# Optimization experiments

Hardware: AMD Instinct MI355X
Metric: run time of the kernel (lower is better)

The kernel has to match this reference:

```python
import jax, jax.numpy as jnp
import numpy as np

D = 1024          # feature_dim
ROT = D // 2      # rotary applied to first feature_dim//2 channels (RotaryEmbedding(dim//2))
B, S = 4, 8192


def _l2norm(x, eps=1e-6):
    # cos_sim feature map: x / ||x||_2 along feature dim
    return x * jax.lax.rsqrt(jnp.sum(x * x, axis=-1, keepdims=True) + eps)


def _rotary(x, rot_dim):
    # lucidrains rotary-embedding-torch: interleaved pairs, partial rotary on first rot_dim dims
    seq = x.shape[-2]
    half = rot_dim // 2
    inv_freq = 1.0 / (10000.0 ** (jnp.arange(0, rot_dim, 2, dtype=jnp.float32) / rot_dim))  # [rot/2]
    freqs = jnp.arange(seq, dtype=jnp.float32)[:, None] * inv_freq[None, :]                  # [s, rot/2]
    freqs = jnp.repeat(freqs, 2, axis=-1)                                                     # [s, rot]
    cos, sin = jnp.cos(freqs), jnp.sin(freqs)
    xr, xp = x[..., :rot_dim], x[..., rot_dim:]
    x2 = xr.reshape(*xr.shape[:-1], half, 2)
    rh = jnp.stack([-x2[..., 1], x2[..., 0]], axis=-1).reshape(xr.shape)  # rotate_half, interleaved
    return jnp.concatenate([xr * cos + rh * sin, xp], axis=-1)


def _layernorm(x, g, b, eps=1e-5):
    mu = jnp.mean(x, axis=-1, keepdims=True)
    var = jnp.mean(jnp.square(x - mu), axis=-1, keepdims=True)
    return (x - mu) * jax.lax.rsqrt(var + eps) * g + b


def setup_inputs() -> dict:
    key = jax.random.key(0)
    k1, k2, k3 = jax.random.split(key, 3)
    X = jax.random.normal(k1, (B, S, D), jnp.float32)
    W_in = jax.random.normal(k2, (3 * D, D), jnp.float32) / np.float32(np.sqrt(D))
    W_out = jax.random.normal(k3, (D, D), jnp.float32) / np.float32(np.sqrt(D))
    ln_g = jnp.ones((D,), jnp.float32)
    ln_b = jnp.zeros((D,), jnp.float32)
    return {"X": X, "W_in": W_in, "W_out": W_out, "ln_g": ln_g, "ln_b": ln_b}


def reference(X, W_in, W_out, ln_g, ln_b):
    Xn = _layernorm(X, ln_g, ln_b)
    QKV = jnp.einsum('bsd,ed->bse', Xn, W_in)        # in_proj, no bias
    Q, K, V = jnp.split(QKV, 3, axis=-1)
    Q = _rotary(Q, ROT)
    K = _rotary(K, ROT)
    A = jnp.sum(_l2norm(K) * V, axis=-2)             # [b, d] global feature-map reduction
    Y = A[:, None, :] * _l2norm(Q)                   # feature_map_attn = identity
    Y = jnp.einsum('bsd,ed->bse', Y, W_out)          # out_proj, no bias
    return Y + X                                     # residual
```

## Files before the change

kernel.cpp:

```cpp
#include <hip/hip_runtime.h>

#define D 1024
#define S_LEN 8192
#define BATCH 4
#define NROWS (BATCH * S_LEN)

typedef unsigned short u16;
typedef __attribute__((ext_vector_type(8))) short short8;
typedef __attribute__((ext_vector_type(8))) unsigned short u16x8;
typedef __attribute__((ext_vector_type(4))) unsigned short u16x4;
typedef __attribute__((ext_vector_type(4))) float f32x4;

__device__ __forceinline__ float bf2f(u16 u) {
  return __builtin_bit_cast(float, ((unsigned)u) << 16);
}
__device__ __forceinline__ u16 f2bf(float f) {
  unsigned u = __builtin_bit_cast(unsigned, f);
  u += 0x7FFFu + ((u >> 16) & 1u);
  return (u16)(u >> 16);
}

#define GLD16(gp, lp)                                                    \
  __builtin_amdgcn_global_load_lds(                                      \
      (__attribute__((address_space(1))) void*)(void*)(gp),              \
      (__attribute__((address_space(3))) void*)(void*)(lp), 16, 0, 0)

__global__ __launch_bounds__(256) void tobf16_kernel(
    const float* __restrict__ src, u16* __restrict__ dst, int n4) {
  int t = blockIdx.x * 256 + threadIdx.x;
  if (t < n4) {
    float4 v = *(const float4*)&src[(size_t)t * 4];
    u16x4 o;
    o[0] = f2bf(v.x); o[1] = f2bf(v.y); o[2] = f2bf(v.z); o[3] = f2bf(v.w);
    *(u16x4*)&dst[(size_t)t * 4] = o;
  }
}

__global__ __launch_bounds__(256) void rope_table_kernel(
    float* __restrict__ ct, float* __restrict__ st) {
  int t = blockIdx.x * 256 + threadIdx.x;
  int s = t >> 8, j = t & 255;
  float invf = exp2f((float)j * -0.0519051265f);
  float f = (float)s * invf;
  float sv, cv;
  sincosf(f, &sv, &cv);
  ct[t] = cv;
  st[t] = sv;
}

__global__ __launch_bounds__(256) void ln_kernel(
    const float* __restrict__ X, const float* __restrict__ g,
    const float* __restrict__ bb, u16* __restrict__ Xn) {
  const int wave = threadIdx.x >> 6, lane = threadIdx.x & 63;
  const int row = blockIdx.x * 4 + wave;
  const float* xr = X + (size_t)row * D;
  float4 v[4];
  float s = 0.f, sq = 0.f;
#pragma unroll
  for (int i = 0; i < 4; i++) {
    v[i] = *(const float4*)&xr[lane * 4 + i * 256];
    s += v[i].x + v[i].y + v[i].z + v[i].w;
    sq += v[i].x * v[i].x + v[i].y * v[i].y + v[i].z * v[i].z + v[i].w * v[i].w;
  }
#pragma unroll
  for (int off = 32; off > 0; off >>= 1) {
    s += __shfl_xor(s, off);
    sq += __shfl_xor(sq, off);
  }
  const float mu = s * (1.f / D);
  const float var = sq * (1.f / D) - mu * mu;
  const float rstd = rsqrtf(var + 1e-5f);
#pragma unroll
  for (int i = 0; i < 4; i++) {
    const int c = lane * 4 + i * 256;
    float4 gg = *(const float4*)&g[c];
    float4 bv = *(const float4*)&bb[c];
    u16x4 o;
    o[0] = f2bf((v[i].x - mu) * rstd * gg.x + bv.x);
    o[1] = f2bf((v[i].y - mu) * rstd * gg.y + bv.y);
    o[2] = f2bf((v[i].z - mu) * rstd * gg.z + bv.z);
    o[3] = f2bf((v[i].w - mu) * rstd * gg.w + bv.w);
    *(u16x4*)&Xn[(size_t)row * D + c] = o;
  }
}

template <int EPI>
__global__ __launch_bounds__(256) void gemm_bt(
    const u16* __restrict__ A, const u16* __restrict__ Bm,
    u16* __restrict__ Cbf, const float* __restrict__ Xres,
    float* __restrict__ Cf, int K, int ldc) {
  __shared__ u16 smem[2 * 128 * 64];
  u16* As = smem;
  u16* Bs = smem + 128 * 64;
  const int tid = threadIdx.x;
  const int wave = tid >> 6, lane = tid & 63;
  const int wm = wave >> 1, wn = wave & 1;
  const int l15 = lane & 15, quad = lane >> 4;
  const int m0 = blockIdx.y * 128;
  const int n0 = blockIdx.x * 128;
  const int sw = l15 & 7;

  f32x4 acc[4][4] = {};

  for (int k0 = 0; k0 < K; k0 += 64) {
    __syncthreads();
#pragma unroll
    for (int i = 0; i < 4; i++) {
      const int c = i * 256 + tid;
      const int row = c >> 3;
      const int g = (c & 7) ^ (row & 7);
      GLD16(&A[(size_t)(m0 + row) * K + k0 + g * 8], &As[c * 8]);
      GLD16(&Bm[(size_t)(n0 + row) * K + k0 + g * 8], &Bs[c * 8]);
    }
    __syncthreads();
#pragma unroll
    for (int ks = 0; ks < 2; ks++) {
      short8 af[4], bfr[4];
#pragma unroll
      for (int i = 0; i < 4; i++)
        af[i] = *(const short8*)
            &As[(wm * 64 + i * 16 + l15) * 64 + (((ks * 4 + quad) ^ sw) << 3)];
#pragma unroll
      for (int j = 0; j < 4; j++)
        bfr[j] = *(const short8*)
            &Bs[(wn * 64 + j * 16 + l15) * 64 + (((ks * 4 + quad) ^ sw) << 3)];
#pragma unroll
      for (int i = 0; i < 4; i++)
#pragma unroll
        for (int j = 0; j < 4; j++)
          acc[i][j] = __builtin_amdgcn_mfma_f32_16x16x32_bf16(
              af[i], bfr[j], acc[i][j], 0, 0, 0);
    }
  }

  if constexpr (EPI == 0) {
    __syncthreads();
    u16* my = smem + wave * 4096;
#pragma unroll
    for (int i = 0; i < 4; i++)
#pragma unroll
      for (int j = 0; j < 4; j++)
#pragma unroll
        for (int r = 0; r < 4; r++)
          my[(i * 16 + quad * 4 + r) * 64 + j * 16 + l15] = f2bf(acc[i][j][r]);
    __syncthreads();
#pragma unroll
    for (int t = 0; t < 8; t++) {
      const int flat = t * 512 + lane * 8;
      const int r64 = flat >> 6, c64 = flat & 63;
      *(u16x8*)&Cbf[(size_t)(m0 + wm * 64 + r64) * ldc + n0 + wn * 64 + c64] =
          *(const u16x8*)&my[flat];
    }
  } else {
#pragma unroll
    for (int i = 0; i < 4; i++) {
#pragma unroll
      for (int r = 0; r < 4; r++) {
        const int row = m0 + wm * 64 + i * 16 + quad * 4 + r;
#pragma unroll
        for (int j = 0; j < 4; j++) {
          const int col = n0 + wn * 64 + j * 16 + l15;
          Cf[(size_t)row * ldc + col] =
              acc[i][j][r] + Xres[(size_t)row * ldc + col];
        }
      }
    }
  }
}

__global__ __launch_bounds__(256) void areduce_kernel(
    const u16* __restrict__ QKV, const float* __restrict__ ct,
    const float* __restrict__ st, float* __restrict__ Aout) {
  const int wave = threadIdx.x >> 6, lane = threadIdx.x & 63;
  const int b = blockIdx.x >> 8;
  const int chunk = blockIdx.x & 255;
  const int c0 = lane << 4;
  float acc[16];
#pragma unroll
  for (int i = 0; i < 16; i++) acc[i] = 0.f;

  for (int t = 0; t < 8; t++) {
    const int s = chunk * 32 + wave * 8 + t;
    const size_t base = ((size_t)b * S_LEN + s) * (3 * D);
    u16x8 ka = *(const u16x8*)&QKV[base + D + c0];
    u16x8 kb = *(const u16x8*)&QKV[base + D + c0 + 8];
    float kx[16];
#pragma unroll
    for (int i = 0; i < 8; i++) { kx[i] = bf2f(ka[i]); kx[8 + i] = bf2f(kb[i]); }
    if (lane < 32) {
      const int jb = c0 >> 1;
      const float* cp = &ct[(size_t)s * 256 + jb];
      const float* sp = &st[(size_t)s * 256 + jb];
#pragma unroll
      for (int p = 0; p < 8; p++) {
        float cv = cp[p], sv = sp[p];
        float e = kx[2 * p], o = kx[2 * p + 1];
        kx[2 * p] = e * cv - o * sv;
        kx[2 * p + 1] = o * cv + e * sv;
      }
    }
    float sq = 0.f;
#pragma unroll
    for (int i = 0; i < 16; i++) sq += kx[i] * kx[i];
#pragma unroll
    for (int off = 32; off > 0; off >>= 1) sq += __shfl_xor(sq, off);
    const float rn = rsqrtf(sq + 1e-6f);
    u16x8 va = *(const u16x8*)&QKV[base + 2 * D + c0];
    u16x8 vb = *(const u16x8*)&QKV[base + 2 * D + c0 + 8];
#pragma unroll
    for (int i = 0; i < 8; i++) {
      acc[i] += kx[i] * rn * bf2f(va[i]);
      acc[8 + i] += kx[8 + i] * rn * bf2f(vb[i]);
    }
  }

  __shared__ float red[D];
  if (wave == 0) {
#pragma unroll
    for (int i = 0; i < 16; i++) red[c0 + i] = acc[i];
  }
  __syncthreads();
  for (int w = 1; w < 4; w++) {
    if (wave == w) {
#pragma unroll
      for (int i = 0; i < 16; i++) red[c0 + i] += acc[i];
    }
    __syncthreads();
  }
  const int tid = threadIdx.x;
#pragma unroll
  for (int i = 0; i < 4; i++)
    atomicAdd(&Aout[(b << 10) + tid * 4 + i], red[tid * 4 + i]);
}

__global__ __launch_bounds__(256) void y_kernel(
    const u16* __restrict__ QKV, const float* __restrict__ ct,
    const float* __restrict__ st, const float* __restrict__ Ain,
    u16* __restrict__ Y) {
  const int wave = threadIdx.x >> 6, lane = threadIdx.x & 63;
  const int row = blockIdx.x * 4 + wave;
  const int b = row >> 13, s = row & (S_LEN - 1);
  const int c0 = lane << 4;
  const size_t base = (size_t)row * (3 * D);
  u16x8 qa = *(const u16x8*)&QKV[base + c0];
  u16x8 qb = *(const u16x8*)&QKV[base + c0 + 8];
  float qx[16];
#pragma unroll
  for (int i = 0; i < 8; i++) { qx[i] = bf2f(qa[i]); qx[8 + i] = bf2f(qb[i]); }
  if (lane < 32) {
    const int jb = c0 >> 1;
    const float* cp = &ct[(size_t)s * 256 + jb];
    const float* sp = &st[(size_t)s * 256 + jb];
#pragma unroll
    for (int p = 0; p < 8; p++) {
      float cv = cp[p], sv = sp[p];
      float e = qx[2 * p], o = qx[2 * p + 1];
      qx[2 * p] = e * cv - o * sv;
      qx[2 * p + 1] = o * cv + e * sv;
    }
  }
  float sq = 0.f;
#pragma unroll
  for (int i = 0; i < 16; i++) sq += qx[i] * qx[i];
#pragma unroll
  for (int off = 32; off > 0; off >>= 1) sq += __shfl_xor(sq, off);
  const float rn = rsqrtf(sq + 1e-6f);
  u16x8 oa, ob;
#pragma unroll
  for (int i = 0; i < 8; i++) {
    oa[i] = f2bf(Ain[(b << 10) + c0 + i] * qx[i] * rn);
    ob[i] = f2bf(Ain[(b << 10) + c0 + 8 + i] * qx[8 + i] * rn);
  }
  *(u16x8*)&Y[(size_t)row * D + c0] = oa;
  *(u16x8*)&Y[(size_t)row * D + c0 + 8] = ob;
}

extern "C" void kernel_launch(void* const* d_in, const int* in_sizes, int n_in,
                              void* d_out, int out_size, void* d_ws, size_t ws_size,
                              hipStream_t stream) {
  const float* X = (const float*)d_in[0];
  const float* W_in = (const float*)d_in[1];
  const float* W_out = (const float*)d_in[2];
  const float* ln_g = (const float*)d_in[3];
  const float* ln_b = (const float*)d_in[4];
  float* out = (float*)d_out;

  char* ws = (char*)d_ws;
  size_t off = 0;
  auto alloc = [&](size_t bytes) -> void* {
    void* p = ws + off;
    off += (bytes + 255) & ~(size_t)255;
    return p;
  };
  u16* QKV = (u16*)alloc((size_t)NROWS * 3 * D * 2);
  u16* Xn = (u16*)alloc((size_t)NROWS * D * 2);
  u16* Yb = (u16*)alloc((size_t)NROWS * D * 2);
  u16* Winb = (u16*)alloc((size_t)3 * D * D * 2);
  u16* Woutb = (u16*)alloc((size_t)D * D * 2);
  float* ct = (float*)alloc((size_t)S_LEN * 256 * 4);
  float* st = (float*)alloc((size_t)S_LEN * 256 * 4);
  float* Aacc = (float*)alloc((size_t)BATCH * D * 4);

  hipMemsetAsync(Aacc, 0, (size_t)BATCH * D * 4, stream);
  tobf16_kernel<<<3 * D * D / 1024, 256, 0, stream>>>(W_in, Winb, 3 * D * D / 4);
  tobf16_kernel<<<D * D / 1024, 256, 0, stream>>>(W_out, Woutb, D * D / 4);
  rope_table_kernel<<<S_LEN, 256, 0, stream>>>(ct, st);
  ln_kernel<<<NROWS / 4, 256, 0, stream>>>(X, ln_g, ln_b, Xn);

  dim3 g1(3 * D / 128, NROWS / 128);
  gemm_bt<0><<<g1, 256, 0, stream>>>(Xn, Winb, QKV, nullptr, nullptr, D, 3 * D);

  areduce_kernel<<<BATCH * 256, 256, 0, stream>>>(QKV, ct, st, Aacc);
  y_kernel<<<NROWS / 4, 256, 0, stream>>>(QKV, ct, st, Aacc, Yb);

  dim3 g2(D / 128, NROWS / 128);
  gemm_bt<1><<<g2, 256, 0, stream>>>(Yb, Woutb, nullptr, X, out, D, D);
}
```

Measured before the change: 670.5 us.

## Coalesce GEMM residual epilogue via LDS, merge weight casts, stagger atomics

The out-projection epilogue now stages fp32 accumulators through shared memory in two halves, so the residual read and output write use contiguous float4 accesses instead of scattered scalar ones. The two weight bf16 conversion launches are merged into one, GEMM load addresses are precomputed and advanced by pointer increments, and the A-reduction atomics start at a per-block offset to spread contention. The costs are extra LDS traffic and an added barrier before the epilogue.

```diff
diff --git a/kernel.cpp b/kernel.cpp
--- a/kernel.cpp
+++ b/kernel.cpp
@@ -26,14 +26,24 @@
       (__attribute__((address_space(3))) void*)(void*)(lp), 16, 0, 0)
 
 __global__ __launch_bounds__(256) void tobf16_kernel(
-    const float* __restrict__ src, u16* __restrict__ dst, int n4) {
+    const float* __restrict__ a, u16* __restrict__ da, int n4a,
+    const float* __restrict__ b, u16* __restrict__ db, int n4b) {
   int t = blockIdx.x * 256 + threadIdx.x;
-  if (t < n4) {
-    float4 v = *(const float4*)&src[(size_t)t * 4];
-    u16x4 o;
-    o[0] = f2bf(v.x); o[1] = f2bf(v.y); o[2] = f2bf(v.z); o[3] = f2bf(v.w);
-    *(u16x4*)&dst[(size_t)t * 4] = o;
-  }
+  const float* s;
+  u16* d;
+  if (t < n4a) {
+    s = a + (size_t)t * 4;
+    d = da + (size_t)t * 4;
+  } else {
+    t -= n4a;
+    if (t >= n4b) return;
+    s = b + (size_t)t * 4;
+    d = db + (size_t)t * 4;
+  }
+  float4 v = *(const float4*)s;
+  u16x4 o;
+  o[0] = f2bf(v.x); o[1] = f2bf(v.y); o[2] = f2bf(v.z); o[3] = f2bf(v.w);
+  *(u16x4*)d = o;
 }
 
 __global__ __launch_bounds__(256) void rope_table_kernel(
@@ -100,17 +110,27 @@
   const int n0 = blockIdx.x * 128;
   const int sw = l15 & 7;
 
+  const u16* pa[4];
+  const u16* pb[4];
+#pragma unroll
+  for (int i = 0; i < 4; i++) {
+    const int c = i * 256 + tid;
+    const int row = c >> 3;
+    const int g = (c & 7) ^ (row & 7);
+    pa[i] = &A[(size_t)(m0 + row) * K + g * 8];
+    pb[i] = &Bm[(size_t)(n0 + row) * K + g * 8];
+  }
+
   f32x4 acc[4][4] = {};
 
   for (int k0 = 0; k0 < K; k0 += 64) {
     __syncthreads();
 #pragma unroll
     for (int i = 0; i < 4; i++) {
-      const int c = i * 256 + tid;
-      const int row = c >> 3;
-      const int g = (c & 7) ^ (row & 7);
-      GLD16(&A[(size_t)(m0 + row) * K + k0 + g * 8], &As[c * 8]);
-      GLD16(&Bm[(size_t)(n0 + row) * K + k0 + g * 8], &Bs[c * 8]);
+      GLD16(pa[i], &As[(i * 256 + tid) * 8]);
+      GLD16(pb[i], &Bs[(i * 256 + tid) * 8]);
+      pa[i] += 64;
+      pb[i] += 64;
     }
     __syncthreads();
 #pragma unroll
@@ -133,8 +153,8 @@
     }
   }
 
+  __syncthreads();
   if constexpr (EPI == 0) {
-    __syncthreads();
     u16* my = smem + wave * 4096;
 #pragma unroll
     for (int i = 0; i < 4; i++)
@@ -152,17 +172,29 @@
           *(const u16x8*)&my[flat];
     }
   } else {
-#pragma unroll
-    for (int i = 0; i < 4; i++) {
-#pragma unroll
-      for (int r = 0; r < 4; r++) {
-        const int row = m0 + wm * 64 + i * 16 + quad * 4 + r;
-#pragma unroll
-        for (int j = 0; j < 4; j++) {
-          const int col = n0 + wn * 64 + j * 16 + l15;
-          Cf[(size_t)row * ldc + col] =
-              acc[i][j][r] + Xres[(size_t)row * ldc + col];
-        }
+    float* fs = (float*)smem + wave * 2048;
+#pragma unroll
+    for (int h = 0; h < 2; h++) {
+#pragma unroll
+      for (int i = 0; i < 4; i++)
+#pragma unroll
+        for (int jj = 0; jj < 2; jj++)
+#pragma unroll
+          for (int r = 0; r < 4; r++)
+            fs[(i * 16 + quad * 4 + r) * 32 + jj * 16 + l15] =
+                acc[i][h * 2 + jj][r];
+#pragma unroll
+      for (int t = 0; t < 8; t++) {
+        const int f = t * 256 + lane * 4;
+        const int r64 = f >> 5, c32 = f & 31;
+        float4 v = *(const float4*)&fs[f];
+        const size_t row = m0 + wm * 64 + r64;
+        const size_t col = n0 + wn * 64 + h * 32 + c32;
+        float4 xr = *(const float4*)&Xres[row * ldc + col];
+        float4 o;
+        o.x = v.x + xr.x; o.y = v.y + xr.y;
+        o.z = v.z + xr.z; o.w = v.w + xr.w;
+        *(float4*)&Cf[row * ldc + col] = o;
       }
     }
   }
@@ -228,9 +260,10 @@
     __syncthreads();
   }
   const int tid = threadIdx.x;
+  const int start = (tid + blockIdx.x * 4) & 255;
 #pragma unroll
   for (int i = 0; i < 4; i++)
-    atomicAdd(&Aout[(b << 10) + tid * 4 + i], red[tid * 4 + i]);
+    atomicAdd(&Aout[(b << 10) + start * 4 + i], red[start * 4 + i]);
 }
 
 __global__ __launch_bounds__(256) void y_kernel(
@@ -302,8 +335,9 @@
   float* Aacc = (float*)alloc((size_t)BATCH * D * 4);
 
   hipMemsetAsync(Aacc, 0, (size_t)BATCH * D * 4, stream);
-  tobf16_kernel<<<3 * D * D / 1024, 256, 0, stream>>>(W_in, Winb, 3 * D * D / 4);
-  tobf16_kernel<<<D * D / 1024, 256, 0, stream>>>(W_out, Woutb, D * D / 4);
+  const int n4a = 3 * D * D / 4, n4b = D * D / 4;
+  tobf16_kernel<<<(n4a + n4b + 255) / 256, 256, 0, stream>>>(W_in, Winb, n4a,
+                                                             W_out, Woutb, n4b);
   rope_table_kernel<<<S_LEN, 256, 0, stream>>>(ct, st);
   ln_kernel<<<NROWS / 4, 256, 0, stream>>>(X, ln_g, ln_b, Xn);
 
```

After: 688.6 us. +2.7%, slower.
